# Kernel tuning notes

Hardware: AMD Instinct MI355X
Metric: run time of the kernel (lower is better)

The kernel has to match this reference:

```python
import jax, jax.numpy as jnp
import numpy as np
from jax import lax

EPS = 0.1        # entropic regularization
MAX_ITER = 100   # Sinkhorn iteration budget
THRESH = 0.1     # early-stop threshold on err = mean_b sum_i |u - u_prev|
B, N, D = 16, 1024, 64


def setup_inputs() -> dict:
    key = jax.random.key(0)
    k1, k2 = jax.random.split(key)
    x = jax.random.normal(k1, (B, N, D), dtype=jnp.float32)
    y = jax.random.normal(k2, (B, N, D), dtype=jnp.float32)
    return {"x": x, "y": y}


def _lse(A):
    # Faithful to the original (unstabilized) lse: log(sum(exp(A)) + 1e-6)
    return jnp.log(jnp.exp(A).sum(-1) + 1e-6)


def _M(C, u, v):
    # (-C_ij + u_i + v_j) / eps
    return (-C + u[..., :, None] + v[..., None, :]) / EPS


def _cost_matrix(x, y):
    # (avoids materializing the [B, N, N, D] difference tensor; same math for p=2)
    x2 = (x * x).sum(-1)                         # [B, N]
    y2 = (y * y).sum(-1)                         # [B, N]
    xy = jnp.einsum('bid,bjd->bij', x, y)        # [B, N, N]
    return x2[..., :, None] + y2[..., None, :] - 2.0 * xy


def reference(x, y):
    x = jax.nn.softmax(x, axis=-1)
    y = jax.nn.softmax(y, axis=-1)
    C = _cost_matrix(x, y)                       # [B, N, N]
    n = x.shape[-2]
    log_mu = jnp.log(1.0 / n + 1e-8)             # mu = nu = uniform 1/n (scalar broadcast)
    u0 = jnp.zeros((x.shape[0], n), dtype=C.dtype)
    v0 = jnp.zeros_like(u0)

    def cond(carry):
        _, _, i, err = carry
        return jnp.logical_and(i < MAX_ITER, err >= THRESH)

    def body(carry):
        u, v, i, _ = carry
        u1 = u
        u = EPS * (log_mu - _lse(_M(C, u, v))) + u
        v = EPS * (log_mu - _lse(jnp.swapaxes(_M(C, u, v), -2, -1))) + v
        err = jnp.abs(u - u1).sum(-1).mean()
        return (u, v, i + 1, err)

    u, v, _, _ = lax.while_loop(
        cond, body, (u0, v0, jnp.int32(0), jnp.float32(jnp.inf)))

    pi = jnp.exp(_M(C, u, v))                    # transport plan [B, N, N]
    cost = (pi * C).sum((-2, -1))                # [B]
    return cost.mean()                           # reduction='mean'
```

## Files before the change

kernel.cpp:

```cpp
#include <hip/hip_runtime.h>
#include <hip/hip_bf16.h>
#include <math.h>

#define BATCH 16
#define NPTS 1024
#define DIM 64
#define EPSF 0.1f
#define INV_EPS 10.0f
#define MAX_ITER 100
#define THRESHF 0.1f
#define LSTRIDE 72

typedef _Float16 h8 __attribute__((ext_vector_type(8)));
typedef short short8v __attribute__((ext_vector_type(8)));
typedef float float4v __attribute__((ext_vector_type(4)));

#define ATOMIC_ST(p, v) \
  __hip_atomic_store((p), (v), __ATOMIC_RELAXED, __HIP_MEMORY_SCOPE_AGENT)
#define ATOMIC_LD(p) \
  __hip_atomic_load((p), __ATOMIC_RELAXED, __HIP_MEMORY_SCOPE_AGENT)

__device__ inline float waveSum(float x) {
#pragma unroll
  for (int off = 32; off; off >>= 1) x += __shfl_xor(x, off, 64);
  return x;
}
__device__ inline float waveMax(float x) {
#pragma unroll
  for (int off = 32; off; off >>= 1) x = fmaxf(x, __shfl_xor(x, off, 64));
  return x;
}

__global__ __launch_bounds__(512, 2) void sinkhorn_fused(
    const float* __restrict__ x, const float* __restrict__ y,
    __hip_bfloat16* __restrict__ syh,
    float* __restrict__ y2,
    float* __restrict__ colsum,
    long long* __restrict__ flags,
    float* __restrict__ errB,
    float* __restrict__ costPart,
    float* __restrict__ out) {
  __shared__ __attribute__((aligned(16))) short xs[64 * LSTRIDE];
  __shared__ __attribute__((aligned(16))) short ys[2][64 * LSTRIDE];
  __shared__ __attribute__((aligned(16))) short os[2][64 * LSTRIDE];
  __shared__ __attribute__((aligned(16))) float wLDS[NPTS];
  __shared__ __attribute__((aligned(16))) float colpart[8][NPTS];
  __shared__ float x2L[64];
  __shared__ float derr[8];
  __shared__ float errbL[BATCH];
  const int t = threadIdx.x;
  const int blk = blockIdx.x;
  const int wave = t >> 6, lane = t & 63;
  const int batch = (blk & 7) + 8 * (blk >> 7);
  const int kslot = (blk >> 3) & 15;
  const float log_mu = logf(1.0f / 1024.0f + 1e-8f);
  const float mu_c = 1.0f / 1024.0f + 1e-8f;

#pragma unroll
  for (int rr = 0; rr < 8; rr++) {
    int rl = wave * 8 + rr;
    int gr = batch * NPTS + kslot * 64 + rl;
    float xv = x[(size_t)gr * DIM + lane];
    float mx = waveMax(xv);
    float ex = __expf(xv - mx);
    float sx = waveSum(ex);
    float px = ex / sx;
    __hip_bfloat16 hbx = (__hip_bfloat16)px;
    xs[rl * LSTRIDE + lane] = *(const short*)&hbx;
    float sqx = waveSum(px * px);
    if (lane == 0) x2L[rl] = sqx;
    float yv = y[(size_t)gr * DIM + lane];
    float my = waveMax(yv);
    float ey = __expf(yv - my);
    float sy = waveSum(ey);
    float py = ey / sy;
    __hip_bfloat16 hby = (__hip_bfloat16)py;
    unsigned bits = *(const unsigned short*)&hby;
    unsigned nb = __shfl_down(bits, 1);
    if ((lane & 1) == 0)
      ATOMIC_ST((unsigned*)((unsigned short*)syh + (size_t)gr * DIM + lane),
                bits | (nb << 16));
    float sqy = waveSum(py * py);
    if (lane == 0) ATOMIC_ST(&y2[gr], sqy);
  }
  if (t < 192) {
    int buf = t >> 6, j = kslot * 64 + (t & 63);
    ATOMIC_ST(&colsum[((size_t)buf * BATCH + batch) * NPTS + j], 0.f);
  }
  __syncthreads();
  if (t == 0) ATOMIC_ST(&flags[batch * 16 + kslot], (long long)1 << 32);
  if (t < 16) {
    while ((int)(ATOMIC_LD(&flags[batch * 16 + t]) >> 32) < 1) {}
  }
  __syncthreads();

  const int m = lane & 15, q = lane >> 4;
  const int g = lane >> 3, sub = lane & 7;
  const int sw = wave & 3, ts = wave >> 2;
  short8v a0 = *(const short8v*)&xs[(sw * 16 + m) * LSTRIDE + q * 8];
  short8v a1 = *(const short8v*)&xs[(sw * 16 + m) * LSTRIDE + 32 + q * 8];
  float xa[4];
#pragma unroll
  for (int reg = 0; reg < 4; reg++) xa[reg] = x2L[sw * 16 + q * 4 + reg];
  float kaf[8][16];
#pragma unroll
  for (int k = 0; k < 8; k++) {
    {
      int idx = t;
#pragma unroll
      for (int rep = 0; rep < 2; rep++, idx += 512) {
        int r = idx >> 3, c = idx & 7;
        *(short8v*)&ys[r >> 6][(r & 63) * LSTRIDE + c * 8] = *(const short8v*)(
            (const short*)syh + ((size_t)batch * NPTS + 128 * k + r) * DIM + c * 8);
      }
    }
    __syncthreads();
    const int jt = 2 * k + ts;
    float4v accv[4];
#pragma unroll
    for (int tj = 0; tj < 4; tj++) {
      short8v b0 = *(const short8v*)&ys[ts][(tj * 16 + m) * LSTRIDE + q * 8];
      short8v b1 = *(const short8v*)&ys[ts][(tj * 16 + m) * LSTRIDE + 32 + q * 8];
      float4v c = {0.f, 0.f, 0.f, 0.f};
      c = __builtin_amdgcn_mfma_f32_16x16x32_bf16(a0, b0, c, 0, 0, 0);
      c = __builtin_amdgcn_mfma_f32_16x16x32_bf16(a1, b1, c, 0, 0, 0);
      accv[tj] = c;
    }
#pragma unroll
    for (int tj = 0; tj < 4; tj++) {
      float y2v = y2[(size_t)batch * NPTS + jt * 64 + tj * 16 + m];
#pragma unroll
      for (int reg = 0; reg < 4; reg++) {
        float C = xa[reg] + y2v - 2.0f * accv[tj][reg];
        _Float16 kv = (_Float16)__expf(-INV_EPS * C);
        os[ts][(sw * 16 + q * 4 + reg) * LSTRIDE + tj * 16 + m] = *(const short*)&kv;
      }
    }
    __syncthreads();
    {
      int e0 = (2 * k) & 7, e1 = (2 * k + 1) & 7;
      if (g == e0 || g == e1) {
        const short* srcp = (g == e0) ? &os[0][0] : &os[1][0];
#pragma unroll
        for (int rr = 0; rr < 8; rr++) {
          h8 v = *(const h8*)&srcp[(wave * 8 + rr) * LSTRIDE + sub * 8];
#pragma unroll
          for (int n = 0; n < 8; n++) {
            if (k < 4) kaf[rr][n] = (float)v[n];
            else kaf[rr][8 + n] = (float)v[n];
          }
        }
      }
    }
    __syncthreads();
  }

  for (int j = t; j < NPTS; j += 512) wLDS[j] = 1.f;
  __syncthreads();

  float eu[8], euPrev[8];
#pragma unroll
  for (int r = 0; r < 8; r++) eu[r] = 1.f;
  int it = 0;

  while (true) {
#pragma unroll
    for (int r = 0; r < 8; r++) euPrev[r] = eu[r];
    const float4* w4 = (const float4*)wLDS;
    float wreg[16];
    *(float4*)&wreg[0]  = w4[2 * lane];
    *(float4*)&wreg[4]  = w4[2 * lane + 1];
    *(float4*)&wreg[8]  = w4[128 + 2 * lane];
    *(float4*)&wreg[12] = w4[128 + 2 * lane + 1];
    float colreg[16];
#pragma unroll
    for (int n = 0; n < 16; n++) colreg[n] = 0.f;
    float delta = 0.f;
#pragma unroll
    for (int rr = 0; rr < 8; rr++) {
      float dot = 0.f;
#pragma unroll
      for (int n = 0; n < 16; n++) dot = fmaf(kaf[rr][n], wreg[n], dot);
      dot = waveSum(dot);
      float sp = eu[rr] * dot + 1e-6f;
      float lg = __logf(sp);
      delta += fabsf(EPSF * (log_mu - lg));
      float ai = mu_c * eu[rr] * __builtin_amdgcn_rcpf(sp);
      eu[rr] = ai;
#pragma unroll
      for (int n = 0; n < 16; n++) colreg[n] = fmaf(kaf[rr][n], ai, colreg[n]);
    }
    if (lane == 0) derr[wave] = delta;
    {
      float4* cp = (float4*)&colpart[wave][0];
      cp[2 * lane]       = make_float4(colreg[0], colreg[1], colreg[2], colreg[3]);
      cp[2 * lane + 1]   = make_float4(colreg[4], colreg[5], colreg[6], colreg[7]);
      cp[128 + 2 * lane] = make_float4(colreg[8], colreg[9], colreg[10], colreg[11]);
      cp[128 + 2 * lane + 1] = make_float4(colreg[12], colreg[13], colreg[14], colreg[15]);
    }
    __syncthreads();
    float* cs = colsum + ((size_t)(it % 3) * BATCH + batch) * NPTS;
    {
      int j0 = (t + (kslot << 6)) & 1023;
      int j1 = j0 ^ 512;
      float s0 = 0.f, s1 = 0.f;
#pragma unroll
      for (int w = 0; w < 8; w++) { s0 += colpart[w][j0]; s1 += colpart[w][j1]; }
      unsafeAtomicAdd(&cs[j0], s0);
      unsafeAtomicAdd(&cs[j1], s1);
    }
    if (it >= 1 && t < BATCH) {
      float v;
      while ((v = ATOMIC_LD(&errB[(it - 1) * BATCH + t])) < 0.f) {}
      errbL[t] = v;
    }
    float eblk = 0.f;
    if (t == 0) {
#pragma unroll
      for (int w = 0; w < 8; w++) eblk += derr[w];
    }
    __syncthreads();
    if (t == 0)
      ATOMIC_ST(&flags[batch * 16 + kslot],
                ((long long)(it + 2) << 32) | (long long)__float_as_uint(eblk));
    if (it >= 1) {
      float errv = 0.f;
#pragma unroll
      for (int k = 0; k < BATCH; k++) errv += errbL[k];
      if (errv * (1.0f / (float)BATCH) < THRESHF) {
#pragma unroll
        for (int r = 0; r < 8; r++) eu[r] = euPrev[r];
        break;
      }
    }
    float dpoll = 0.f;
    if (t < 16) {
      long long fw;
      while ((int)((fw = ATOMIC_LD(&flags[batch * 16 + t])) >> 32) < it + 2) {}
      dpoll = __uint_as_float((unsigned)fw);
    }
    __syncthreads();
    float cs0 = ATOMIC_LD(&cs[t]);
    float cs1 = ATOMIC_LD(&cs[t + 512]);
    if (t < 64)
      ATOMIC_ST(&colsum[((size_t)((it + 2) % 3) * BATCH + batch) * NPTS +
                        kslot * 64 + t], 0.f);
    if (wave == 0) {
      float e16 = (lane < 16) ? dpoll : 0.f;
#pragma unroll
      for (int off = 8; off; off >>= 1) e16 += __shfl_xor(e16, off, 16);
      if (t == 0 && kslot == 0) ATOMIC_ST(&errB[it * BATCH + batch], e16);
    }
    {
      float w0 = wLDS[t];
      wLDS[t] = mu_c * w0 * __builtin_amdgcn_rcpf(w0 * cs0 + 1e-6f);
      float w1 = wLDS[t + 512];
      wLDS[t + 512] = mu_c * w1 * __builtin_amdgcn_rcpf(w1 * cs1 + 1e-6f);
    }
    it++;
    if (it >= MAX_ITER) break;
    __syncthreads();
  }

  {
    __syncthreads();
    const float4* w4 = (const float4*)wLDS;
    float wreg[16];
    *(float4*)&wreg[0]  = w4[2 * lane];
    *(float4*)&wreg[4]  = w4[2 * lane + 1];
    *(float4*)&wreg[8]  = w4[128 + 2 * lane];
    *(float4*)&wreg[12] = w4[128 + 2 * lane + 1];
    float csum = 0.f;
#pragma unroll
    for (int rr = 0; rr < 8; rr++) {
      float ai = eu[rr];
#pragma unroll
      for (int n = 0; n < 16; n++) {
        float kf = kaf[rr][n];
        if (kf > 0.f)
          csum += ai * wreg[n] * kf * (-EPSF * __logf(kf));
      }
    }
    csum = waveSum(csum);
    if (lane == 0) derr[wave] = csum;
    __syncthreads();
    if (t == 0) {
      float cst = 0.f;
#pragma unroll
      for (int w = 0; w < 8; w++) cst += derr[w];
      ATOMIC_ST(&costPart[blk], cst + 1.0f);
    }
    if (blk == 0) {
      if (t < 256) {
        float v;
        while ((v = ATOMIC_LD(&costPart[t])) < 0.5f) {}
        colpart[0][t] = v;
      }
      __syncthreads();
      if (wave == 0) {
        float s = colpart[0][lane] + colpart[0][lane + 64] +
                  colpart[0][lane + 128] + colpart[0][lane + 192];
        s = waveSum(s);
        if (lane == 0) out[0] = (s - 256.0f) * (1.0f / (float)BATCH);
      }
    }
  }
}

extern "C" void kernel_launch(void* const* d_in, const int* in_sizes, int n_in,
                              void* d_out, int out_size, void* d_ws,
                              size_t ws_size, hipStream_t stream) {
  (void)in_sizes; (void)n_in; (void)out_size; (void)ws_size;
  const float* x = (const float*)d_in[0];
  const float* y = (const float*)d_in[1];
  float* out = (float*)d_out;

  char* ws = (char*)d_ws;
  size_t off = 0;
  auto alloc = [&](size_t nbytes) -> void* {
    void* p = (void*)(ws + off);
    off = (off + nbytes + 255) & ~(size_t)255;
    return p;
  };
  __hip_bfloat16* syh = (__hip_bfloat16*)alloc((size_t)BATCH * NPTS * DIM * 2);
  float* y2 = (float*)alloc((size_t)BATCH * NPTS * 4);
  float* colsum = (float*)alloc((size_t)3 * BATCH * NPTS * 4);
  long long* flags = (long long*)alloc((size_t)BATCH * 16 * 8);
  float* errB = (float*)alloc((size_t)MAX_ITER * BATCH * 4);
  float* costPart = (float*)alloc(256 * 4);

  void* args[] = {&x, &y, &syh, &y2, &colsum, &flags,
                  &errB, &costPart, &out};
  hipLaunchCooperativeKernel((void*)sinkhorn_fused, dim3(256), dim3(512), args,
                             0, stream);
}
```

Before: 131.6 us.

## Replace atomic-add column sums with tagged partial exchange and reduce-scatter

Each block used to atomically add its column partial sums into a shared triple-buffered colsum array, then wait on per-block flags. Now each block writes its partials as tag+value 64-bit words. Each block then polls and reduces the 16 partials for its own 64-column slice and publishes a tagged column sum that all blocks poll. This removes atomic-add contention, buffer zeroing and the separate flag barrier. In exchange it adds two rounds of polling latency and more global traffic per iteration.

```diff
diff --git a/kernel.cpp b/kernel.cpp
--- a/kernel.cpp
+++ b/kernel.cpp
@@ -30,12 +30,22 @@
   for (int off = 32; off; off >>= 1) x = fmaxf(x, __shfl_xor(x, off, 64));
   return x;
 }
+__device__ inline long long packTag(int tag, float v) {
+  return ((long long)tag << 32) | (long long)__float_as_uint(v);
+}
+__device__ inline long long pollTag(long long* p, int tag) {
+  long long w;
+  do { w = ATOMIC_LD(p); } while ((int)(w >> 32) < tag);
+  return w;
+}
 
 __global__ __launch_bounds__(512, 2) void sinkhorn_fused(
     const float* __restrict__ x, const float* __restrict__ y,
     __hip_bfloat16* __restrict__ syh,
     float* __restrict__ y2,
-    float* __restrict__ colsum,
+    long long* __restrict__ partialT,
+    long long* __restrict__ csT,
+    long long* __restrict__ deltaT,
     long long* __restrict__ flags,
     float* __restrict__ errB,
     float* __restrict__ costPart,
@@ -45,6 +55,7 @@
   __shared__ __attribute__((aligned(16))) short os[2][64 * LSTRIDE];
   __shared__ __attribute__((aligned(16))) float wLDS[NPTS];
   __shared__ __attribute__((aligned(16))) float colpart[8][NPTS];
+  __shared__ __attribute__((aligned(16))) float red[16][66];
   __shared__ float x2L[64];
   __shared__ float derr[8];
   __shared__ float errbL[BATCH];
@@ -83,10 +94,6 @@
     float sqy = waveSum(py * py);
     if (lane == 0) ATOMIC_ST(&y2[gr], sqy);
   }
-  if (t < 192) {
-    int buf = t >> 6, j = kslot * 64 + (t & 63);
-    ATOMIC_ST(&colsum[((size_t)buf * BATCH + batch) * NPTS + j], 0.f);
-  }
   __syncthreads();
   if (t == 0) ATOMIC_ST(&flags[batch * 16 + kslot], (long long)1 << 32);
   if (t < 16) {
@@ -162,6 +169,11 @@
 #pragma unroll
   for (int r = 0; r < 8; r++) eu[r] = 1.f;
   int it = 0;
+
+  const int oks = t >> 5;
+  const int oc = (t & 31) * 2;
+  long long* opT =
+      &partialT[(((size_t)batch * 16 + oks) << 10) + kslot * 64 + oc];
 
   while (true) {
 #pragma unroll
@@ -199,30 +211,27 @@
       cp[128 + 2 * lane + 1] = make_float4(colreg[12], colreg[13], colreg[14], colreg[15]);
     }
     __syncthreads();
-    float* cs = colsum + ((size_t)(it % 3) * BATCH + batch) * NPTS;
-    {
-      int j0 = (t + (kslot << 6)) & 1023;
-      int j1 = j0 ^ 512;
+    {
       float s0 = 0.f, s1 = 0.f;
 #pragma unroll
-      for (int w = 0; w < 8; w++) { s0 += colpart[w][j0]; s1 += colpart[w][j1]; }
-      unsafeAtomicAdd(&cs[j0], s0);
-      unsafeAtomicAdd(&cs[j1], s1);
+      for (int w = 0; w < 8; w++) { s0 += colpart[w][t]; s1 += colpart[w][t + 512]; }
+      long long* wp = &partialT[(((size_t)batch * 16 + kslot) << 10) + t];
+      ATOMIC_ST(wp, packTag(it + 2, s0));
+      ATOMIC_ST(wp + 512, packTag(it + 2, s1));
+    }
+    if (t == 0) {
+      float e = 0.f;
+#pragma unroll
+      for (int w = 0; w < 8; w++) e += derr[w];
+      ATOMIC_ST(&deltaT[((it & 1) * BATCH + batch) * 16 + kslot],
+                packTag(it + 2, e));
     }
     if (it >= 1 && t < BATCH) {
       float v;
       while ((v = ATOMIC_LD(&errB[(it - 1) * BATCH + t])) < 0.f) {}
       errbL[t] = v;
     }
-    float eblk = 0.f;
-    if (t == 0) {
-#pragma unroll
-      for (int w = 0; w < 8; w++) eblk += derr[w];
-    }
-    __syncthreads();
-    if (t == 0)
-      ATOMIC_ST(&flags[batch * 16 + kslot],
-                ((long long)(it + 2) << 32) | (long long)__float_as_uint(eblk));
+    __syncthreads();
     if (it >= 1) {
       float errv = 0.f;
 #pragma unroll
@@ -233,23 +242,38 @@
         break;
       }
     }
-    float dpoll = 0.f;
-    if (t < 16) {
-      long long fw;
-      while ((int)((fw = ATOMIC_LD(&flags[batch * 16 + t])) >> 32) < it + 2) {}
-      dpoll = __uint_as_float((unsigned)fw);
-    }
-    __syncthreads();
-    float cs0 = ATOMIC_LD(&cs[t]);
-    float cs1 = ATOMIC_LD(&cs[t + 512]);
-    if (t < 64)
-      ATOMIC_ST(&colsum[((size_t)((it + 2) % 3) * BATCH + batch) * NPTS +
-                        kslot * 64 + t], 0.f);
-    if (wave == 0) {
-      float e16 = (lane < 16) ? dpoll : 0.f;
+    {
+      long long w0 = pollTag(opT, it + 2);
+      long long w1 = pollTag(opT + 1, it + 2);
+      red[oks][oc] = __uint_as_float((unsigned)w0);
+      red[oks][oc + 1] = __uint_as_float((unsigned)w1);
+    }
+    __syncthreads();
+    if (t < 64) {
+      float s = 0.f;
+#pragma unroll
+      for (int k2 = 0; k2 < 16; k2++) s += red[k2][t];
+      ATOMIC_ST(&csT[((size_t)batch << 10) + kslot * 64 + t],
+                packTag(it + 2, s));
+    }
+    if (kslot == 0 && wave == 0) {
+      float e16 = 0.f;
+      if (lane < 16) {
+        long long fw =
+            pollTag(&deltaT[((it & 1) * BATCH + batch) * 16 + lane], it + 2);
+        e16 = __uint_as_float((unsigned)fw);
+      }
 #pragma unroll
       for (int off = 8; off; off >>= 1) e16 += __shfl_xor(e16, off, 16);
-      if (t == 0 && kslot == 0) ATOMIC_ST(&errB[it * BATCH + batch], e16);
+      if (lane == 0) ATOMIC_ST(&errB[it * BATCH + batch], e16);
+    }
+    float cs0, cs1;
+    {
+      long long* cp0 = &csT[((size_t)batch << 10) + t];
+      long long a = pollTag(cp0, it + 2);
+      long long b = pollTag(cp0 + 512, it + 2);
+      cs0 = __uint_as_float((unsigned)a);
+      cs1 = __uint_as_float((unsigned)b);
     }
     {
       float w0 = wLDS[t];
@@ -324,13 +348,15 @@
   };
   __hip_bfloat16* syh = (__hip_bfloat16*)alloc((size_t)BATCH * NPTS * DIM * 2);
   float* y2 = (float*)alloc((size_t)BATCH * NPTS * 4);
-  float* colsum = (float*)alloc((size_t)3 * BATCH * NPTS * 4);
+  long long* partialT = (long long*)alloc((size_t)BATCH * 16 * NPTS * 8);
+  long long* csT = (long long*)alloc((size_t)BATCH * NPTS * 8);
+  long long* deltaT = (long long*)alloc((size_t)2 * BATCH * 16 * 8);
   long long* flags = (long long*)alloc((size_t)BATCH * 16 * 8);
   float* errB = (float*)alloc((size_t)MAX_ITER * BATCH * 4);
   float* costPart = (float*)alloc(256 * 4);
 
-  void* args[] = {&x, &y, &syh, &y2, &colsum, &flags,
-                  &errB, &costPart, &out};
+  void* args[] = {&x, &y, &syh, &y2, &partialT, &csT, &deltaT,
+                  &flags, &errB, &costPart, &out};
   hipLaunchCooperativeKernel((void*)sinkhorn_fused, dim3(256), dim3(512), args,
                              0, stream);
 }
```

Measured after the change: 132.7 us. No clear change (+0.8%).

## Interleave two batches per block and use packed fp16 dot products in Sinkhorn loop

Applied to the files above, without the earlier changes.

Each block now owns 32 rows from each of two batches instead of 64 rows of one, so every Sinkhorn iteration alternates two independent sub-problems. One batch's atomic colsum reduction and flag polling overlap with the other batch's compute. The kernel matrix stays in fp16 registers and the row dot products and column accumulations use packed half2 fdot2 and fma with scaled fp16 weights. This halves register use for K and hides cross-block sync latency, at the cost of fp16 accumulation precision, an extra flag array and doubled LDS buffers.

```diff
diff --git a/kernel.cpp b/kernel.cpp
--- a/kernel.cpp
+++ b/kernel.cpp
@@ -12,8 +12,14 @@
 #define LSTRIDE 72
 
 typedef _Float16 h8 __attribute__((ext_vector_type(8)));
+typedef _Float16 half2v __attribute__((ext_vector_type(2)));
 typedef short short8v __attribute__((ext_vector_type(8)));
 typedef float float4v __attribute__((ext_vector_type(4)));
+
+template <int P>
+__device__ __forceinline__ half2v h2get(h8 v) {
+  return __builtin_shufflevector(v, v, 2 * P, 2 * P + 1);
+}
 
 #define ATOMIC_ST(p, v) \
   __hip_atomic_store((p), (v), __ATOMIC_RELAXED, __HIP_MEMORY_SCOPE_AGENT)
@@ -30,232 +36,307 @@
   for (int off = 32; off; off >>= 1) x = fmaxf(x, __shfl_xor(x, off, 64));
   return x;
 }
+__device__ inline long long packTag(int tag, float v) {
+  return ((long long)tag << 32) | (long long)__float_as_uint(v);
+}
+__device__ inline long long pollTag(long long* p, int tag) {
+  long long w;
+  do { w = ATOMIC_LD(p); } while ((int)(w >> 32) < tag);
+  return w;
+}
+
+#define DOT8(P, KAr, KBr)                                                   \
+  d0 = __builtin_amdgcn_fdot2(h2get<P>(KAr), h2get<P>(wh0), d0, false);     \
+  d1 = __builtin_amdgcn_fdot2(h2get<P>(KBr), h2get<P>(wh1), d1, false);
+#define PKF(P, KAr, KBr)                                                    \
+  c0[P] = h2get<P>(KAr) * ai2 + c0[P];                                      \
+  c1[P] = h2get<P>(KBr) * ai2 + c1[P];
+#define PHASEA_ROW(KAr, KBr, EUr)                                           \
+  {                                                                         \
+    float d0 = 0.f, d1 = 0.f;                                               \
+    DOT8(0, KAr, KBr) DOT8(1, KAr, KBr) DOT8(2, KAr, KBr) DOT8(3, KAr, KBr) \
+    float dot = waveSum(d0 + d1);                                           \
+    float sp = (EUr) * dot + 1e-6f;                                         \
+    float lg = __logf(sp);                                                  \
+    delta += fabsf(EPSF * (log_mu - lg));           \
+    float ai = mu_c * (EUr) * __builtin_amdgcn_rcpf(sp);                    \
+    (EUr) = ai;                                                             \
+    _Float16 aih = (_Float16)(ai * 1024.0f);                                \
+    half2v ai2 = {aih, aih};                                                \
+    PKF(0, KAr, KBr) PKF(1, KAr, KBr) PKF(2, KAr, KBr) PKF(3, KAr, KBr)     \
+  }
+#define PHASEA(WH, KAa, KBa, EUa, CP, DERR)                                 \
+  {                                                                         \
+    h8 wh0 = *(const h8*)&WH[8 * lane];                                     \
+    h8 wh1 = *(const h8*)&WH[512 + 8 * lane];                               \
+    half2v c0[4], c1[4];                                                    \
+    c0[0] = c0[1] = c0[2] = c0[3] = half2v{(_Float16)0.f, (_Float16)0.f};   \
+    c1[0] = c1[1] = c1[2] = c1[3] = half2v{(_Float16)0.f, (_Float16)0.f};   \
+    float delta = 0.f;                                                      \
+    PHASEA_ROW(KAa[0], KBa[0], EUa[0])                                      \
+    PHASEA_ROW(KAa[1], KBa[1], EUa[1])                                      \
+    PHASEA_ROW(KAa[2], KBa[2], EUa[2])                                      \
+    PHASEA_ROW(KAa[3], KBa[3], EUa[3])                                      \
+    if (lane == 0) DERR[wave] = delta;                                      \
+    float4* cp = (float4*)&CP[wave][0];                                     \
+    cp[2 * lane] = make_float4((float)c0[0][0], (float)c0[0][1],            \
+                               (float)c0[1][0], (float)c0[1][1]);           \
+    cp[2 * lane + 1] = make_float4((float)c0[2][0], (float)c0[2][1],        \
+                                   (float)c0[3][0], (float)c0[3][1]);       \
+    cp[128 + 2 * lane] = make_float4((float)c1[0][0], (float)c1[0][1],      \
+                                     (float)c1[1][0], (float)c1[1][1]);     \
+    cp[128 + 2 * lane + 1] = make_float4((float)c1[2][0], (float)c1[2][1],  \
+                                         (float)c1[3][0], (float)c1[3][1]); \
+  }
 
 __global__ __launch_bounds__(512, 2) void sinkhorn_fused(
     const float* __restrict__ x, const float* __restrict__ y,
     __hip_bfloat16* __restrict__ syh,
     float* __restrict__ y2,
     float* __restrict__ colsum,
-    long long* __restrict__ flags,
+    long long* __restrict__ fA,
+    long long* __restrict__ fB,
     float* __restrict__ errB,
     float* __restrict__ costPart,
     float* __restrict__ out) {
   __shared__ __attribute__((aligned(16))) short xs[64 * LSTRIDE];
   __shared__ __attribute__((aligned(16))) short ys[2][64 * LSTRIDE];
-  __shared__ __attribute__((aligned(16))) short os[2][64 * LSTRIDE];
-  __shared__ __attribute__((aligned(16))) float wLDS[NPTS];
-  __shared__ __attribute__((aligned(16))) float colpart[8][NPTS];
+  __shared__ __attribute__((aligned(16))) short os[2][32 * LSTRIDE];
+  __shared__ __attribute__((aligned(16))) float wLA[NPTS];
+  __shared__ __attribute__((aligned(16))) float wLB[NPTS];
+  __shared__ __attribute__((aligned(16))) _Float16 whA[NPTS];
+  __shared__ __attribute__((aligned(16))) _Float16 whB[NPTS];
+  __shared__ __attribute__((aligned(16))) float cpA[8][NPTS];
+  __shared__ __attribute__((aligned(16))) float cpB[8][NPTS];
   __shared__ float x2L[64];
-  __shared__ float derr[8];
+  __shared__ float derrA[8], derrB[8];
   __shared__ float errbL[BATCH];
   const int t = threadIdx.x;
   const int blk = blockIdx.x;
   const int wave = t >> 6, lane = t & 63;
-  const int batch = (blk & 7) + 8 * (blk >> 7);
-  const int kslot = (blk >> 3) & 15;
+  const int bA = blk & 7, bB = bA + 8;
+  const int s = blk >> 3;
   const float log_mu = logf(1.0f / 1024.0f + 1e-8f);
   const float mu_c = 1.0f / 1024.0f + 1e-8f;
 
 #pragma unroll
-  for (int rr = 0; rr < 8; rr++) {
-    int rl = wave * 8 + rr;
-    int gr = batch * NPTS + kslot * 64 + rl;
-    float xv = x[(size_t)gr * DIM + lane];
-    float mx = waveMax(xv);
-    float ex = __expf(xv - mx);
-    float sx = waveSum(ex);
-    float px = ex / sx;
-    __hip_bfloat16 hbx = (__hip_bfloat16)px;
-    xs[rl * LSTRIDE + lane] = *(const short*)&hbx;
-    float sqx = waveSum(px * px);
-    if (lane == 0) x2L[rl] = sqx;
-    float yv = y[(size_t)gr * DIM + lane];
-    float my = waveMax(yv);
-    float ey = __expf(yv - my);
-    float sy = waveSum(ey);
-    float py = ey / sy;
-    __hip_bfloat16 hby = (__hip_bfloat16)py;
-    unsigned bits = *(const unsigned short*)&hby;
-    unsigned nb = __shfl_down(bits, 1);
-    if ((lane & 1) == 0)
-      ATOMIC_ST((unsigned*)((unsigned short*)syh + (size_t)gr * DIM + lane),
-                bits | (nb << 16));
-    float sqy = waveSum(py * py);
-    if (lane == 0) ATOMIC_ST(&y2[gr], sqy);
+  for (int sl = 0; sl < 2; sl++) {
+    int b = sl ? bB : bA;
+#pragma unroll
+    for (int rr = 0; rr < 4; rr++) {
+      int rl = wave * 4 + rr;
+      int gr = b * NPTS + s * 32 + rl;
+      float xv = x[(size_t)gr * DIM + lane];
+      float mx = waveMax(xv);
+      float ex = __expf(xv - mx);
+      float sx = waveSum(ex);
+      float px = ex / sx;
+      __hip_bfloat16 hbx = (__hip_bfloat16)px;
+      xs[(sl * 32 + rl) * LSTRIDE + lane] = *(const short*)&hbx;
+      float sqx = waveSum(px * px);
+      if (lane == 0) x2L[sl * 32 + rl] = sqx;
+      float yv = y[(size_t)gr * DIM + lane];
+      float my = waveMax(yv);
+      float ey = __expf(yv - my);
+      float sy = waveSum(ey);
+      float py = ey / sy;
+      __hip_bfloat16 hby = (__hip_bfloat16)py;
+      unsigned bits = *(const unsigned short*)&hby;
+      unsigned nb = __shfl_down(bits, 1);
+      if ((lane & 1) == 0)
+        ATOMIC_ST((unsigned*)((unsigned short*)syh + (size_t)gr * DIM + lane),
+                  bits | (nb << 16));
+      float sqy = waveSum(py * py);
+      if (lane == 0) ATOMIC_ST(&y2[gr], sqy);
+    }
   }
   if (t < 192) {
-    int buf = t >> 6, j = kslot * 64 + (t & 63);
-    ATOMIC_ST(&colsum[((size_t)buf * BATCH + batch) * NPTS + j], 0.f);
+    int buf = t >> 6, r = t & 63, sl = r >> 5, c = r & 31;
+    int b = sl ? bB : bA;
+    ATOMIC_ST(&colsum[((size_t)buf * BATCH + b) * NPTS + s * 32 + c], 0.f);
   }
   __syncthreads();
-  if (t == 0) ATOMIC_ST(&flags[batch * 16 + kslot], (long long)1 << 32);
-  if (t < 16) {
-    while ((int)(ATOMIC_LD(&flags[batch * 16 + t]) >> 32) < 1) {}
+  if (t == 0) ATOMIC_ST(&fA[bA * 32 + s], (long long)1 << 32);
+  if (t < 32) {
+    while ((int)(ATOMIC_LD(&fA[bA * 32 + t]) >> 32) < 1) {}
   }
   __syncthreads();
 
   const int m = lane & 15, q = lane >> 4;
   const int g = lane >> 3, sub = lane & 7;
-  const int sw = wave & 3, ts = wave >> 2;
-  short8v a0 = *(const short8v*)&xs[(sw * 16 + m) * LSTRIDE + q * 8];
-  short8v a1 = *(const short8v*)&xs[(sw * 16 + m) * LSTRIDE + 32 + q * 8];
-  float xa[4];
-#pragma unroll
-  for (int reg = 0; reg < 4; reg++) xa[reg] = x2L[sw * 16 + q * 4 + reg];
-  float kaf[8][16];
-#pragma unroll
-  for (int k = 0; k < 8; k++) {
-    {
-      int idx = t;
-#pragma unroll
-      for (int rep = 0; rep < 2; rep++, idx += 512) {
-        int r = idx >> 3, c = idx & 7;
-        *(short8v*)&ys[r >> 6][(r & 63) * LSTRIDE + c * 8] = *(const short8v*)(
-            (const short*)syh + ((size_t)batch * NPTS + 128 * k + r) * DIM + c * 8);
-      }
-    }
-    __syncthreads();
-    const int jt = 2 * k + ts;
-    float4v accv[4];
-#pragma unroll
-    for (int tj = 0; tj < 4; tj++) {
-      short8v b0 = *(const short8v*)&ys[ts][(tj * 16 + m) * LSTRIDE + q * 8];
-      short8v b1 = *(const short8v*)&ys[ts][(tj * 16 + m) * LSTRIDE + 32 + q * 8];
-      float4v c = {0.f, 0.f, 0.f, 0.f};
-      c = __builtin_amdgcn_mfma_f32_16x16x32_bf16(a0, b0, c, 0, 0, 0);
-      c = __builtin_amdgcn_mfma_f32_16x16x32_bf16(a1, b1, c, 0, 0, 0);
-      accv[tj] = c;
-    }
-#pragma unroll
-    for (int tj = 0; tj < 4; tj++) {
-      float y2v = y2[(size_t)batch * NPTS + jt * 64 + tj * 16 + m];
-#pragma unroll
-      for (int reg = 0; reg < 4; reg++) {
-        float C = xa[reg] + y2v - 2.0f * accv[tj][reg];
-        _Float16 kv = (_Float16)__expf(-INV_EPS * C);
-        os[ts][(sw * 16 + q * 4 + reg) * LSTRIDE + tj * 16 + m] = *(const short*)&kv;
-      }
-    }
-    __syncthreads();
-    {
-      int e0 = (2 * k) & 7, e1 = (2 * k + 1) & 7;
-      if (g == e0 || g == e1) {
-        const short* srcp = (g == e0) ? &os[0][0] : &os[1][0];
-#pragma unroll
-        for (int rr = 0; rr < 8; rr++) {
-          h8 v = *(const h8*)&srcp[(wave * 8 + rr) * LSTRIDE + sub * 8];
-#pragma unroll
-          for (int n = 0; n < 8; n++) {
-            if (k < 4) kaf[rr][n] = (float)v[n];
-            else kaf[rr][8 + n] = (float)v[n];
+  const int sw2 = wave & 1, q4 = wave >> 1;
+  h8 kaA[4], kbA[4], kaB[4], kbB[4];
+#pragma unroll
+  for (int sl = 0; sl < 2; sl++) {
+    int b = sl ? bB : bA;
+    short8v a0 = *(const short8v*)&xs[(sl * 32 + sw2 * 16 + m) * LSTRIDE + q * 8];
+    short8v a1 = *(const short8v*)&xs[(sl * 32 + sw2 * 16 + m) * LSTRIDE + 32 + q * 8];
+    float xa[4];
+#pragma unroll
+    for (int reg = 0; reg < 4; reg++)
+      xa[reg] = x2L[sl * 32 + sw2 * 16 + q * 4 + reg];
+#pragma unroll
+    for (int k = 0; k < 8; k++) {
+      {
+        int idx = t;
+#pragma unroll
+        for (int rep = 0; rep < 2; rep++, idx += 512) {
+          int r = idx >> 3, c = idx & 7;
+          *(short8v*)&ys[r >> 6][(r & 63) * LSTRIDE + c * 8] = *(const short8v*)(
+              (const short*)syh + ((size_t)b * NPTS + 128 * k + r) * DIM + c * 8);
+        }
+      }
+      __syncthreads();
+#pragma unroll
+      for (int tjq = 0; tjq < 2; tjq++) {
+        int jcol = q4 * 32 + tjq * 16 + m;
+        short8v b0 = *(const short8v*)&ys[jcol >> 6][(jcol & 63) * LSTRIDE + q * 8];
+        short8v b1 = *(const short8v*)&ys[jcol >> 6][(jcol & 63) * LSTRIDE + 32 + q * 8];
+        float4v c = {0.f, 0.f, 0.f, 0.f};
+        c = __builtin_amdgcn_mfma_f32_16x16x32_bf16(a0, b0, c, 0, 0, 0);
+        c = __builtin_amdgcn_mfma_f32_16x16x32_bf16(a1, b1, c, 0, 0, 0);
+        float y2v = y2[(size_t)b * NPTS + 128 * k + jcol];
+#pragma unroll
+        for (int reg = 0; reg < 4; reg++) {
+          float C = xa[reg] + y2v - 2.0f * c[reg];
+          _Float16 kv = (_Float16)__expf(-INV_EPS * C);
+          os[jcol >> 6][(sw2 * 16 + q * 4 + reg) * LSTRIDE + (jcol & 63)] =
+              *(const short*)&kv;
+        }
+      }
+      __syncthreads();
+      {
+        int e0 = (2 * k) & 7, e1 = (2 * k + 1) & 7;
+        if (g == e0 || g == e1) {
+          const short* srcp = (g == e0) ? &os[0][0] : &os[1][0];
+#pragma unroll
+          for (int rr = 0; rr < 4; rr++) {
+            h8 v = *(const h8*)&srcp[(wave * 4 + rr) * LSTRIDE + sub * 8];
+            if (sl == 0) {
+              if (k < 4) kaA[rr] = v; else kbA[rr] = v;
+            } else {
+              if (k < 4) kaB[rr] = v; else kbB[rr] = v;
+            }
           }
         }
       }
-    }
-    __syncthreads();
-  }
-
-  for (int j = t; j < NPTS; j += 512) wLDS[j] = 1.f;
+      __syncthreads();
+    }
+  }
+
+  for (int j = t; j < NPTS; j += 512) {
+    wLA[j] = 1.f; wLB[j] = 1.f;
+    whA[j] = (_Float16)1.f; whB[j] = (_Float16)1.f;
+  }
   __syncthreads();
 
-  float eu[8], euPrev[8];
-#pragma unroll
-  for (int r = 0; r < 8; r++) eu[r] = 1.f;
+  float euA[4], euB[4], epA[4], epB[4];
+#pragma unroll
+  for (int r = 0; r < 4; r++) { euA[r] = 1.f; euB[r] = 1.f; }
   int it = 0;
+  const int j0 = (t + s * 32) & 1023, j1 = j0 ^ 512;
 
   while (true) {
 #pragma unroll
-    for (int r = 0; r < 8; r++) euPrev[r] = eu[r];
-    const float4* w4 = (const float4*)wLDS;
-    float wreg[16];
-    *(float4*)&wreg[0]  = w4[2 * lane];
-    *(float4*)&wreg[4]  = w4[2 * lane + 1];
-    *(float4*)&wreg[8]  = w4[128 + 2 * lane];
-    *(float4*)&wreg[12] = w4[128 + 2 * lane + 1];
-    float colreg[16];
-#pragma unroll
-    for (int n = 0; n < 16; n++) colreg[n] = 0.f;
-    float delta = 0.f;
-#pragma unroll
-    for (int rr = 0; rr < 8; rr++) {
-      float dot = 0.f;
-#pragma unroll
-      for (int n = 0; n < 16; n++) dot = fmaf(kaf[rr][n], wreg[n], dot);
-      dot = waveSum(dot);
-      float sp = eu[rr] * dot + 1e-6f;
-      float lg = __logf(sp);
-      delta += fabsf(EPSF * (log_mu - lg));
-      float ai = mu_c * eu[rr] * __builtin_amdgcn_rcpf(sp);
-      eu[rr] = ai;
-#pragma unroll
-      for (int n = 0; n < 16; n++) colreg[n] = fmaf(kaf[rr][n], ai, colreg[n]);
-    }
-    if (lane == 0) derr[wave] = delta;
-    {
-      float4* cp = (float4*)&colpart[wave][0];
-      cp[2 * lane]       = make_float4(colreg[0], colreg[1], colreg[2], colreg[3]);
-      cp[2 * lane + 1]   = make_float4(colreg[4], colreg[5], colreg[6], colreg[7]);
-      cp[128 + 2 * lane] = make_float4(colreg[8], colreg[9], colreg[10], colreg[11]);
-      cp[128 + 2 * lane + 1] = make_float4(colreg[12], colreg[13], colreg[14], colreg[15]);
-    }
-    __syncthreads();
-    float* cs = colsum + ((size_t)(it % 3) * BATCH + batch) * NPTS;
-    {
-      int j0 = (t + (kslot << 6)) & 1023;
-      int j1 = j0 ^ 512;
+    for (int r = 0; r < 4; r++) { epA[r] = euA[r]; epB[r] = euB[r]; }
+    PHASEA(whA, kaA, kbA, euA, cpA, derrA)
+    __syncthreads();
+    {
+      float* cs = colsum + ((size_t)(it % 3) * BATCH + bA) * NPTS;
       float s0 = 0.f, s1 = 0.f;
 #pragma unroll
-      for (int w = 0; w < 8; w++) { s0 += colpart[w][j0]; s1 += colpart[w][j1]; }
+      for (int w = 0; w < 8; w++) { s0 += cpA[w][j0]; s1 += cpA[w][j1]; }
       unsafeAtomicAdd(&cs[j0], s0);
       unsafeAtomicAdd(&cs[j1], s1);
     }
+    PHASEA(whB, kaB, kbB, euB, cpB, derrB)
     if (it >= 1 && t < BATCH) {
       float v;
       while ((v = ATOMIC_LD(&errB[(it - 1) * BATCH + t])) < 0.f) {}
       errbL[t] = v;
     }
-    float eblk = 0.f;
+    __syncthreads();
     if (t == 0) {
-#pragma unroll
-      for (int w = 0; w < 8; w++) eblk += derr[w];
-    }
-    __syncthreads();
-    if (t == 0)
-      ATOMIC_ST(&flags[batch * 16 + kslot],
-                ((long long)(it + 2) << 32) | (long long)__float_as_uint(eblk));
+      float e = 0.f;
+#pragma unroll
+      for (int w = 0; w < 8; w++) e += derrA[w];
+      ATOMIC_ST(&fA[bA * 32 + s], packTag(it + 2, e));
+    }
+    {
+      float* cs = colsum + ((size_t)(it % 3) * BATCH + bB) * NPTS;
+      float s0 = 0.f, s1 = 0.f;
+#pragma unroll
+      for (int w = 0; w < 8; w++) { s0 += cpB[w][j0]; s1 += cpB[w][j1]; }
+      unsafeAtomicAdd(&cs[j0], s0);
+      unsafeAtomicAdd(&cs[j1], s1);
+    }
     if (it >= 1) {
       float errv = 0.f;
 #pragma unroll
       for (int k = 0; k < BATCH; k++) errv += errbL[k];
       if (errv * (1.0f / (float)BATCH) < THRESHF) {
 #pragma unroll
-        for (int r = 0; r < 8; r++) eu[r] = euPrev[r];
+        for (int r = 0; r < 4; r++) { euA[r] = epA[r]; euB[r] = epB[r]; }
         break;
       }
     }
-    float dpoll = 0.f;
-    if (t < 16) {
-      long long fw;
-      while ((int)((fw = ATOMIC_LD(&flags[batch * 16 + t])) >> 32) < it + 2) {}
-      dpoll = __uint_as_float((unsigned)fw);
-    }
-    __syncthreads();
-    float cs0 = ATOMIC_LD(&cs[t]);
-    float cs1 = ATOMIC_LD(&cs[t + 512]);
-    if (t < 64)
-      ATOMIC_ST(&colsum[((size_t)((it + 2) % 3) * BATCH + batch) * NPTS +
-                        kslot * 64 + t], 0.f);
-    if (wave == 0) {
-      float e16 = (lane < 16) ? dpoll : 0.f;
-#pragma unroll
-      for (int off = 8; off; off >>= 1) e16 += __shfl_xor(e16, off, 16);
-      if (t == 0 && kslot == 0) ATOMIC_ST(&errB[it * BATCH + batch], e16);
-    }
-    {
-      float w0 = wLDS[t];
-      wLDS[t] = mu_c * w0 * __builtin_amdgcn_rcpf(w0 * cs0 + 1e-6f);
-      float w1 = wLDS[t + 512];
-      wLDS[t + 512] = mu_c * w1 * __builtin_amdgcn_rcpf(w1 * cs1 + 1e-6f);
+    float dpA = 0.f;
+    if (t < 32)
+      dpA = __uint_as_float((unsigned)pollTag(&fA[bA * 32 + t], it + 2));
+    __syncthreads();
+    if (t == 0) {
+      float e = 0.f;
+#pragma unroll
+      for (int w = 0; w < 8; w++) e += derrB[w];
+      ATOMIC_ST(&fB[bA * 32 + s], packTag(it + 2, e));
+    }
+    const float* csA = colsum + ((size_t)(it % 3) * BATCH + bA) * NPTS;
+    float a0v = ATOMIC_LD((float*)&csA[t]);
+    float a1v = ATOMIC_LD((float*)&csA[t + 512]);
+    if (t < 32)
+      ATOMIC_ST(&colsum[((size_t)((it + 2) % 3) * BATCH + bA) * NPTS + s * 32 + t],
+                0.f);
+    float dpB = 0.f;
+    if (t < 32)
+      dpB = __uint_as_float((unsigned)pollTag(&fB[bA * 32 + t], it + 2));
+    if (wave == 0 && s == 0) {
+      float e = (lane < 32) ? dpA : 0.f;
+#pragma unroll
+      for (int off = 16; off; off >>= 1) e += __shfl_xor(e, off, 32);
+      if (lane == 0) ATOMIC_ST(&errB[it * BATCH + bA], e);
+    }
+    __syncthreads();
+    const float* csB = colsum + ((size_t)(it % 3) * BATCH + bB) * NPTS;
+    float b0v = ATOMIC_LD((float*)&csB[t]);
+    float b1v = ATOMIC_LD((float*)&csB[t + 512]);
+    if (t < 32)
+      ATOMIC_ST(&colsum[((size_t)((it + 2) % 3) * BATCH + bB) * NPTS + s * 32 + t],
+                0.f);
+    {
+      float w0 = wLA[t];
+      float wn0 = mu_c * w0 *
+                  __builtin_amdgcn_rcpf(w0 * a0v + (1e-6f * 1024.0f)) * 1024.0f;
+      wLA[t] = wn0; whA[t] = (_Float16)wn0;
+      float w1 = wLA[t + 512];
+      float wn1 = mu_c * w1 *
+                  __builtin_amdgcn_rcpf(w1 * a1v + (1e-6f * 1024.0f)) * 1024.0f;
+      wLA[t + 512] = wn1; whA[t + 512] = (_Float16)wn1;
+    }
+    if (wave == 0 && s == 0) {
+      float e = (lane < 32) ? dpB : 0.f;
+#pragma unroll
+      for (int off = 16; off; off >>= 1) e += __shfl_xor(e, off, 32);
+      if (lane == 0) ATOMIC_ST(&errB[it * BATCH + bB], e);
+    }
+    {
+      float w0 = wLB[t];
+      float wn0 = mu_c * w0 *
+                  __builtin_amdgcn_rcpf(w0 * b0v + (1e-6f * 1024.0f)) * 1024.0f;
+      wLB[t] = wn0; whB[t] = (_Float16)wn0;
+      float w1 = wLB[t + 512];
+      float wn1 = mu_c * w1 *
+                  __builtin_amdgcn_rcpf(w1 * b1v + (1e-6f * 1024.0f)) * 1024.0f;
+      wLB[t + 512] = wn1; whB[t + 512] = (_Float16)wn1;
     }
     it++;
     if (it >= MAX_ITER) break;
@@ -264,44 +345,66 @@
 
   {
     __syncthreads();
-    const float4* w4 = (const float4*)wLDS;
-    float wreg[16];
-    *(float4*)&wreg[0]  = w4[2 * lane];
-    *(float4*)&wreg[4]  = w4[2 * lane + 1];
-    *(float4*)&wreg[8]  = w4[128 + 2 * lane];
-    *(float4*)&wreg[12] = w4[128 + 2 * lane + 1];
     float csum = 0.f;
-#pragma unroll
-    for (int rr = 0; rr < 8; rr++) {
-      float ai = eu[rr];
-#pragma unroll
-      for (int n = 0; n < 16; n++) {
-        float kf = kaf[rr][n];
-        if (kf > 0.f)
-          csum += ai * wreg[n] * kf * (-EPSF * __logf(kf));
+    {
+      const float4* w4 = (const float4*)wLA;
+      float wreg[16];
+      *(float4*)&wreg[0] = w4[2 * lane];
+      *(float4*)&wreg[4] = w4[2 * lane + 1];
+      *(float4*)&wreg[8] = w4[128 + 2 * lane];
+      *(float4*)&wreg[12] = w4[128 + 2 * lane + 1];
+#pragma unroll
+      for (int rr = 0; rr < 4; rr++) {
+        float ai = euA[rr];
+#pragma unroll
+        for (int n = 0; n < 8; n++) {
+          float kf = (float)kaA[rr][n];
+          if (kf > 0.f) csum += ai * wreg[n] * kf * (-EPSF * __logf(kf));
+          float kg = (float)kbA[rr][n];
+          if (kg > 0.f) csum += ai * wreg[8 + n] * kg * (-EPSF * __logf(kg));
+        }
+      }
+    }
+    {
+      const float4* w4 = (const float4*)wLB;
+      float wreg[16];
+      *(float4*)&wreg[0] = w4[2 * lane];
+      *(float4*)&wreg[4] = w4[2 * lane + 1];
+      *(float4*)&wreg[8] = w4[128 + 2 * lane];
+      *(float4*)&wreg[12] = w4[128 + 2 * lane + 1];
+#pragma unroll
+      for (int rr = 0; rr < 4; rr++) {
+        float ai = euB[rr];
+#pragma unroll
+        for (int n = 0; n < 8; n++) {
+          float kf = (float)kaB[rr][n];
+          if (kf > 0.f) csum += ai * wreg[n] * kf * (-EPSF * __logf(kf));
+          float kg = (float)kbB[rr][n];
+          if (kg > 0.f) csum += ai * wreg[8 + n] * kg * (-EPSF * __logf(kg));
+        }
       }
     }
     csum = waveSum(csum);
-    if (lane == 0) derr[wave] = csum;
+    if (lane == 0) derrA[wave] = csum;
     __syncthreads();
     if (t == 0) {
       float cst = 0.f;
 #pragma unroll
-      for (int w = 0; w < 8; w++) cst += derr[w];
+      for (int w = 0; w < 8; w++) cst += derrA[w];
       ATOMIC_ST(&costPart[blk], cst + 1.0f);
     }
     if (blk == 0) {
       if (t < 256) {
         float v;
         while ((v = ATOMIC_LD(&costPart[t])) < 0.5f) {}
-        colpart[0][t] = v;
+        cpA[0][t] = v;
       }
       __syncthreads();
       if (wave == 0) {
-        float s = colpart[0][lane] + colpart[0][lane + 64] +
-                  colpart[0][lane + 128] + colpart[0][lane + 192];
-        s = waveSum(s);
-        if (lane == 0) out[0] = (s - 256.0f) * (1.0f / (float)BATCH);
+        float gv = cpA[0][lane] + cpA[0][lane + 64] + cpA[0][lane + 128] +
+                   cpA[0][lane + 192];
+        gv = waveSum(gv);
+        if (lane == 0) out[0] = (gv - 256.0f) * (1.0f / (float)BATCH);
       }
     }
   }
@@ -325,11 +428,12 @@
   __hip_bfloat16* syh = (__hip_bfloat16*)alloc((size_t)BATCH * NPTS * DIM * 2);
   float* y2 = (float*)alloc((size_t)BATCH * NPTS * 4);
   float* colsum = (float*)alloc((size_t)3 * BATCH * NPTS * 4);
-  long long* flags = (long long*)alloc((size_t)BATCH * 16 * 8);
+  long long* fA = (long long*)alloc((size_t)8 * 32 * 8);
+  long long* fB = (long long*)alloc((size_t)8 * 32 * 8);
   float* errB = (float*)alloc((size_t)MAX_ITER * BATCH * 4);
   float* costPart = (float*)alloc(256 * 4);
 
-  void* args[] = {&x, &y, &syh, &y2, &colsum, &flags,
+  void* args[] = {&x, &y, &syh, &y2, &colsum, &fA, &fB,
                   &errB, &costPart, &out};
   hipLaunchCooperativeKernel((void*)sinkhorn_fused, dim3(256), dim3(512), args,
                              0, stream);
```

New measurement: 137.1 us. 4.2% more time.
